# Kernel optimization log

Hardware: AMD Instinct MI355X
Metric: run time of the kernel (lower is better)

Reference implementation:

```python
import jax, jax.numpy as jnp
import numpy as np
import math

NUM_HEADS = 16


def setup_inputs() -> dict:
    key = jax.random.key(0)
    k0, k1, k2, k3, k4 = jax.random.split(key, 5)
    B, S, D = 2, 2048, 1024
    scale = 1.0 / math.sqrt(D)
    return {
        "x": jax.random.normal(k0, (B, S, D), dtype=jnp.float32),
        "Wq": jax.random.normal(k1, (D, D), dtype=jnp.float32) * scale,
        "Wk": jax.random.normal(k2, (D, D), dtype=jnp.float32) * scale,
        "Wv": jax.random.normal(k3, (D, D), dtype=jnp.float32) * scale,
        "Wo": jax.random.normal(k4, (D, D), dtype=jnp.float32) * scale,
    }


def reference(x, Wq, Wk, Wv, Wo):
    B, S, D = x.shape
    H = NUM_HEADS
    dk = D // H
    # nn.Linear(bias=False): y = x @ W.T; weights stored [out, in]
    def proj(W):
        return jnp.einsum('bsd,ed->bse', x, W).reshape(B, S, H, dk).transpose(0, 2, 1, 3)
    q = proj(Wq)  # [B, H, S, dk]
    k = proj(Wk)
    v = proj(Wv)
    scores = jnp.einsum('bhqd,bhkd->bhqk', q, k) / jnp.sqrt(jnp.float32(dk))
    causal = jnp.tril(jnp.ones((S, S), dtype=bool))  # True = keep
    scores = jnp.where(causal, scores, -jnp.inf)
    attn = jax.nn.softmax(scores, axis=-1)
    out = jnp.einsum('bhqk,bhkd->bhqd', attn, v)  # [B, H, S, dk]
    out = out.transpose(0, 2, 1, 3).reshape(B, S, D)
    return jnp.einsum('bsd,ed->bse', out, Wo)
```

## Files before the change

kernel.cpp:

```cpp
#include <hip/hip_runtime.h>
#include <hip/hip_bf16.h>

#define S_LEN 2048
#define S_PAD 2112
#define D_DIM 1024
#define N_HEADS 16
#define M_ROWS 4096

typedef __bf16 bf16x8 __attribute__((ext_vector_type(8)));
typedef float f32x4 __attribute__((ext_vector_type(4)));
typedef float f32x16 __attribute__((ext_vector_type(16)));
typedef unsigned short ushortx8 __attribute__((ext_vector_type(8)));
typedef unsigned int uintx4 __attribute__((ext_vector_type(4)));

__device__ __forceinline__ unsigned short f2bf(float f) {
  unsigned int u = __builtin_bit_cast(unsigned int, f);
  u += 0x7fffu + ((u >> 16) & 1u);
  return (unsigned short)(u >> 16);
}

__device__ __forceinline__ unsigned int cvtpk(float lo, float hi) {
  unsigned int r;
  asm("v_cvt_pk_bf16_f32 %0, %1, %2" : "=v"(r) : "v"(lo), "v"(hi));
  return r;
}

__device__ __forceinline__ void pl32swap(unsigned int& a, unsigned int& b) {
  asm("v_permlane32_swap_b32 %0, %1" : "+v"(a), "+v"(b));
}

__device__ __forceinline__ bf16x8 load8(const unsigned short* p) {
  return __builtin_bit_cast(bf16x8, *(const ushortx8*)p);
}

__device__ __forceinline__ void gload16(const unsigned short* g, unsigned short* l) {
  __builtin_amdgcn_global_load_lds((const __attribute__((address_space(1))) void*)g,
                                   (__attribute__((address_space(3))) void*)l,
                                   16, 0, 0);
}

__global__ void cvt5_kernel(const float* __restrict__ s0, const float* __restrict__ s1,
                            const float* __restrict__ s2, const float* __restrict__ s3,
                            const float* __restrict__ s4,
                            unsigned short* __restrict__ d0, unsigned short* __restrict__ d1,
                            unsigned short* __restrict__ d2, unsigned short* __restrict__ d3,
                            unsigned short* __restrict__ d4,
                            int n4x, int n4w) {
  const int y = blockIdx.y;
  const float* s = (y == 0) ? s0 : (y == 1) ? s1 : (y == 2) ? s2 : (y == 3) ? s3 : s4;
  unsigned short* d = (y == 0) ? d0 : (y == 1) ? d1 : (y == 2) ? d2 : (y == 3) ? d3 : d4;
  const int n4 = (y == 0) ? n4x : n4w;
  int i = blockIdx.x * blockDim.x + threadIdx.x;
  if (i < n4) {
    float4 f = ((const float4*)s)[i];
    unsigned int u0 = cvtpk(f.x, f.y), u1 = cvtpk(f.z, f.w);
    unsigned long long packed = (unsigned long long)u0 | ((unsigned long long)u1 << 32);
    ((unsigned long long*)d)[i] = packed;
  }
}

__global__ __launch_bounds__(256) void gemm_bt(
    const unsigned short* __restrict__ A,
    const unsigned short* __restrict__ B0,
    const unsigned short* __restrict__ B1,
    const unsigned short* __restrict__ B2,
    void* __restrict__ C0, void* __restrict__ C1, void* __restrict__ C2,
    int M, int N, int K, int modesel)
{
  __shared__ __align__(16) unsigned short At[128 * 64];
  __shared__ __align__(16) unsigned short Bt[128 * 64];

  const int bid = blockIdx.x + 8 * (blockIdx.y + 32 * blockIdx.z);
  const int k8 = bid & 7, t = bid >> 3;
  const int zz = t >> 5;
  const int u = t & 31;
  const int bxi = (k8 & 1) * 4 + (u & 3);
  const int byi = (k8 >> 1) * 8 + (u >> 2);

  const int z = zz;
  const unsigned short* Bp = (z == 0) ? B0 : (z == 1) ? B1 : B2;
  void* Cp = (z == 0) ? C0 : (z == 1) ? C1 : C2;
  const int mode = (modesel == 0) ? 0 : ((z == 2) ? 2 : 1);
  const float escale = (modesel == 1 && z == 0) ? 0.180336879f : 1.0f;

  const int tid = threadIdx.x;
  const int lane = tid & 63, wave = tid >> 6;
  const int bm = byi * 128, bn = bxi * 128;
  const int wr = wave >> 1, wc = wave & 1;
  const int cl = lane & 15, g = lane >> 4;
  const int ci = lane >> 3, si = lane & 7;
  const int sg = si ^ (ci & 7);

  f32x4 acc[4][4] = {};

  for (int kb = 0; kb < K; kb += 64) {
    __syncthreads();
#pragma unroll
    for (int cc = 0; cc < 4; ++cc) {
      int chunk = wave * 4 + cc;
      int row = chunk * 8 + ci;
      gload16(A  + (size_t)(bm + row) * K + kb + sg * 8, &At[chunk * 512]);
      gload16(Bp + (size_t)(bn + row) * K + kb + sg * 8, &Bt[chunk * 512]);
    }
    __syncthreads();
#pragma unroll
    for (int kc = 0; kc < 2; ++kc) {
      bf16x8 af[4], bfr[4];
#pragma unroll
      for (int mi = 0; mi < 4; ++mi) {
        int row = wr * 64 + mi * 16 + cl;
        int slot = (kc * 4 + g) ^ (row & 7);
        af[mi] = load8(&At[row * 64 + slot * 8]);
      }
#pragma unroll
      for (int ni = 0; ni < 4; ++ni) {
        int row = wc * 64 + ni * 16 + cl;
        int slot = (kc * 4 + g) ^ (row & 7);
        bfr[ni] = load8(&Bt[row * 64 + slot * 8]);
      }
#pragma unroll
      for (int mi = 0; mi < 4; ++mi)
#pragma unroll
        for (int ni = 0; ni < 4; ++ni)
          acc[mi][ni] = __builtin_amdgcn_mfma_f32_16x16x32_bf16(af[mi], bfr[ni], acc[mi][ni], 0, 0, 0);
    }
  }

  const int r0 = g * 4;
#pragma unroll
  for (int mi = 0; mi < 4; ++mi) {
#pragma unroll
    for (int ni = 0; ni < 4; ++ni) {
      int mg = bm + wr * 64 + mi * 16 + r0;
      int ng = bn + wc * 64 + ni * 16 + cl;
#pragma unroll
      for (int r = 0; r < 4; ++r) {
        float v = acc[mi][ni][r] * escale;
        int m = mg + r;
        if (mode == 0) {
          ((float*)Cp)[(size_t)m * N + ng] = v;
        } else {
          int b = m >> 11, s = m & 2047;
          int h = ng >> 6, d = ng & 63;
          unsigned short* o = (unsigned short*)Cp;
          if (mode == 1) o[((size_t)(b * N_HEADS + h) * S_LEN + s) * 64 + d] = f2bf(v);
          else           o[((size_t)(b * N_HEADS + h) * 64 + d) * S_PAD + s] = f2bf(v);
        }
      }
    }
  }
}

__global__ __launch_bounds__(256) void gemm_o64(
    const unsigned short* __restrict__ A,
    const unsigned short* __restrict__ B,
    float* __restrict__ C, int M, int N, int K)
{
  __shared__ __align__(16) unsigned short At[64 * 64];
  __shared__ __align__(16) unsigned short Bt[128 * 64];

  const int bid = blockIdx.x;
  const int k8 = bid & 7, t = bid >> 3;
  const int bxi = t & 7;
  const int byi = k8 * 8 + (t >> 3);

  const int tid = threadIdx.x;
  const int lane = tid & 63, wave = tid >> 6;
  const int bm = byi * 64, bn = bxi * 128;
  const int wr = wave >> 1, wc = wave & 1;
  const int cl = lane & 15, g = lane >> 4;
  const int ci = lane >> 3, si = lane & 7;
  const int sg = si ^ (ci & 7);

  f32x4 acc[2][4] = {};

  for (int kb = 0; kb < K; kb += 64) {
    __syncthreads();
#pragma unroll
    for (int cc = 0; cc < 2; ++cc) {
      int chunk = wave * 2 + cc;
      int row = chunk * 8 + ci;
      gload16(A + (size_t)(bm + row) * K + kb + sg * 8, &At[chunk * 512]);
    }
#pragma unroll
    for (int cc = 0; cc < 4; ++cc) {
      int chunk = wave * 4 + cc;
      int row = chunk * 8 + ci;
      gload16(B + (size_t)(bn + row) * K + kb + sg * 8, &Bt[chunk * 512]);
    }
    __syncthreads();
#pragma unroll
    for (int kc = 0; kc < 2; ++kc) {
      bf16x8 af[2], bfr[4];
#pragma unroll
      for (int mi = 0; mi < 2; ++mi) {
        int row = wr * 32 + mi * 16 + cl;
        int slot = (kc * 4 + g) ^ (row & 7);
        af[mi] = load8(&At[row * 64 + slot * 8]);
      }
#pragma unroll
      for (int ni = 0; ni < 4; ++ni) {
        int row = wc * 64 + ni * 16 + cl;
        int slot = (kc * 4 + g) ^ (row & 7);
        bfr[ni] = load8(&Bt[row * 64 + slot * 8]);
      }
#pragma unroll
      for (int mi = 0; mi < 2; ++mi)
#pragma unroll
        for (int ni = 0; ni < 4; ++ni)
          acc[mi][ni] = __builtin_amdgcn_mfma_f32_16x16x32_bf16(af[mi], bfr[ni], acc[mi][ni], 0, 0, 0);
    }
  }

  const int r0 = g * 4;
#pragma unroll
  for (int mi = 0; mi < 2; ++mi)
#pragma unroll
    for (int ni = 0; ni < 4; ++ni) {
      int mg = bm + wr * 32 + mi * 16 + r0;
      int ng = bn + wc * 64 + ni * 16 + cl;
#pragma unroll
      for (int r = 0; r < 4; ++r)
        C[(size_t)(mg + r) * N + ng] = acc[mi][ni][r];
    }
}

__global__ __launch_bounds__(256) void attn_kernel(
    const unsigned short* __restrict__ Qg,
    const unsigned short* __restrict__ Kg,
    const unsigned short* __restrict__ Vtg,
    unsigned short* __restrict__ Og)
{
  __shared__ __align__(16) unsigned short Kb[2][8192];
  __shared__ __align__(16) unsigned short Vb[2][8192];

  const int tid = threadIdx.x;
  const int lane = tid & 63, wave = tid >> 6;
  const int l31 = lane & 31, hi = lane >> 5;

  const int bh = (blockIdx.x & 7) * 4 + ((blockIdx.x >> 3) & 3);
  const int t  = 15 - (blockIdx.x >> 5);
  const int qt = t * 128;
  const size_t qkb = (size_t)bh * S_LEN;
  const int b = bh >> 4, h = bh & 15;

  int cur = 0;

  auto stageK = [&](int buf, int ch) {
    const unsigned short* base = Kg + (qkb + (size_t)ch * 128) * 64;
#pragma unroll
    for (int ii = 0; ii < 4; ++ii) {
      int i = wave * 4 + ii;
      int ri = i * 8 + (lane >> 3);
      int e = (((lane & 7) ^ (lane >> 3)) << 3);
      gload16(base + (size_t)ri * 64 + e, &Kb[buf][i * 512]);
    }
  };
  auto stageV = [&](int buf, int ch) {
    const unsigned short* base = Vtg + (size_t)bh * 64 * S_PAD + ch * 128;
#pragma unroll
    for (int ii = 0; ii < 4; ++ii) {
      int i = wave * 4 + ii;
      int ri = i * 4 + (lane >> 4);
      int e = (((lane & 15) ^ (ri & 7)) << 3);
      gload16(base + (size_t)ri * S_PAD + e, &Vb[buf][i * 512]);
    }
  };

  const int swz = (l31 & 7) << 3;

  auto kblock = [&](int buf, const bf16x8 (&bq)[4], f32x16 (&o)[2], float& lpart,
                    int j, int jj, bool domask, int qrow) {
    bf16x8 kc[4];
    int krow = j * 32 + l31;
#pragma unroll
    for (int f = 0; f < 4; ++f)
      kc[f] = load8(&Kb[buf][krow * 64 + ((f * 16 + hi * 8) ^ swz)]);
    f32x16 c = {};
    __builtin_amdgcn_s_setprio(1);
#pragma unroll
    for (int f = 0; f < 4; ++f)
      c = __builtin_amdgcn_mfma_f32_32x32x16_bf16(kc[f], bq[f], c, 0, 0, 0);
    __builtin_amdgcn_s_setprio(0);
    if (domask) {
#pragma unroll
      for (int r = 0; r < 16; ++r) {
        int k = jj * 32 + (r & 3) + 8 * (r >> 2) + 4 * hi;
        if (k > qrow) c[r] = -1e30f;
      }
    }
    float s0 = 0.f, s1 = 0.f;
#pragma unroll
    for (int r = 0; r < 16; r += 2) {
      c[r] = __builtin_amdgcn_exp2f(c[r]);         s0 += c[r];
      c[r + 1] = __builtin_amdgcn_exp2f(c[r + 1]); s1 += c[r + 1];
    }
    lpart += s0 + s1;
    bf16x8 pb[2];
#pragma unroll
    for (int kf = 0; kf < 2; ++kf) {
      unsigned int x0 = cvtpk(c[8 * kf + 0], c[8 * kf + 1]);
      unsigned int x1 = cvtpk(c[8 * kf + 2], c[8 * kf + 3]);
      unsigned int y0 = cvtpk(c[8 * kf + 4], c[8 * kf + 5]);
      unsigned int y1 = cvtpk(c[8 * kf + 6], c[8 * kf + 7]);
      pl32swap(x0, y0); pl32swap(x1, y1);
      pb[kf] = __builtin_bit_cast(bf16x8, (uintx4){x0, x1, y0, y1});
    }
    bf16x8 vf[2][2];
#pragma unroll
    for (int kf = 0; kf < 2; ++kf)
#pragma unroll
      for (int dt = 0; dt < 2; ++dt)
        vf[kf][dt] = load8(&Vb[buf][(dt * 32 + l31) * 128 + ((j * 32 + kf * 16 + hi * 8) ^ swz)]);
    __builtin_amdgcn_s_setprio(1);
#pragma unroll
    for (int kf = 0; kf < 2; ++kf)
#pragma unroll
      for (int dt = 0; dt < 2; ++dt)
        o[dt] = __builtin_amdgcn_mfma_f32_32x32x16_bf16(vf[kf][dt], pb[kf], o[dt], 0, 0, 0);
    __builtin_amdgcn_s_setprio(0);
  };

  bf16x8 bq[4];
#pragma unroll
  for (int f = 0; f < 4; ++f)
    bq[f] = load8(Qg + (qkb + qt + wave * 32 + l31) * 64 + f * 16 + hi * 8);

  f32x16 o[2] = {};
  float lpart = 0.f;
  const int qrow = qt + wave * 32 + l31;

  stageK(0, 0); stageV(0, 0);
  __syncthreads();

  for (int ch = 0; ch < t; ++ch) {
    stageK(cur ^ 1, ch + 1);
    stageV(cur ^ 1, ch + 1);
#pragma unroll
    for (int j = 0; j < 4; ++j)
      kblock(cur, bq, o, lpart, j, 0, false, 0);
    __syncthreads();
    cur ^= 1;
  }
  for (int j = 0; j <= wave; ++j)
    kblock(cur, bq, o, lpart, j, 4 * t + j, j == wave, qrow);

  {
    float lf = lpart + __shfl_xor(lpart, 32, 64);
    float inv = 1.0f / lf;
    unsigned short* base = Og + ((size_t)(b * S_LEN + qt + wave * 32 + l31)) * D_DIM
                         + h * 64 + 4 * hi;
#pragma unroll
    for (int dt = 0; dt < 2; ++dt)
#pragma unroll
      for (int rc = 0; rc < 4; ++rc) {
        unsigned int u0 = cvtpk(o[dt][4 * rc] * inv, o[dt][4 * rc + 1] * inv);
        unsigned int u1 = cvtpk(o[dt][4 * rc + 2] * inv, o[dt][4 * rc + 3] * inv);
        *(unsigned long long*)&base[dt * 32 + 8 * rc] =
            (unsigned long long)u0 | ((unsigned long long)u1 << 32);
      }
  }
}

extern "C" void kernel_launch(void* const* d_in, const int* in_sizes, int n_in,
                              void* d_out, int out_size, void* d_ws, size_t ws_size,
                              hipStream_t stream) {
  const float* x  = (const float*)d_in[0];
  const float* Wq = (const float*)d_in[1];
  const float* Wk = (const float*)d_in[2];
  const float* Wv = (const float*)d_in[3];
  const float* Wo = (const float*)d_in[4];

  const int M = M_ROWS, D = D_DIM;

  unsigned short* ws  = (unsigned short*)d_ws;
  unsigned short* xb  = ws;
  unsigned short* wqb = xb  + (size_t)M * D;
  unsigned short* wkb = wqb + (size_t)D * D;
  unsigned short* wvb = wkb + (size_t)D * D;
  unsigned short* wob = wvb + (size_t)D * D;
  unsigned short* qb  = wob + (size_t)D * D;
  unsigned short* kbf = qb  + (size_t)M * D;
  unsigned short* vtb = kbf + (size_t)M * D;
  unsigned short* aob = vtb + (size_t)32 * 64 * S_PAD;

  {
    dim3 gc(M * D / 4 / 256, 5);
    cvt5_kernel<<<gc, 256, 0, stream>>>(x, Wq, Wk, Wv, Wo,
                                        xb, wqb, wkb, wvb, wob,
                                        M * D / 4, D * D / 4);
  }

  dim3 gq(8, 32, 3);
  gemm_bt<<<gq, 256, 0, stream>>>(xb, wqb, wkb, wvb, qb, kbf, vtb, M, D, D, 1);

  attn_kernel<<<512, 256, 0, stream>>>(qb, kbf, vtb, aob);

  gemm_o64<<<512, 256, 0, stream>>>(aob, wob, (float*)d_out, M, D, D);
}
```

Before: 108.2 us.

## Double-buffer shared-memory tiles in projection and output GEMMs

Both GEMM kernels now keep two LDS buffers per operand and issue the global-to-LDS loads for the next K tile before computing on the current one. This cuts one barrier per iteration and aims to overlap load latency with MFMA work. It doubles LDS usage (64KB for gemm_bt), which may lower occupancy. Correctness depends on gload16 being a direct-to-LDS async load that completes by the single barrier at the end of each iteration.

Result: slower. 113.0 us (+4.4%).

```diff
diff --git a/kernel.cpp b/kernel.cpp
--- a/kernel.cpp
+++ b/kernel.cpp
@@ -67,8 +67,8 @@
     void* __restrict__ C0, void* __restrict__ C1, void* __restrict__ C2,
     int M, int N, int K, int modesel)
 {
-  __shared__ __align__(16) unsigned short At[128 * 64];
-  __shared__ __align__(16) unsigned short Bt[128 * 64];
+  __shared__ __align__(16) unsigned short At[2][128 * 64];
+  __shared__ __align__(16) unsigned short Bt[2][128 * 64];
 
   const int bid = blockIdx.x + 8 * (blockIdx.y + 32 * blockIdx.z);
   const int k8 = bid & 7, t = bid >> 3;
@@ -93,16 +93,23 @@
 
   f32x4 acc[4][4] = {};
 
-  for (int kb = 0; kb < K; kb += 64) {
-    __syncthreads();
+  auto stage = [&](int buf, int kb) {
 #pragma unroll
     for (int cc = 0; cc < 4; ++cc) {
       int chunk = wave * 4 + cc;
       int row = chunk * 8 + ci;
-      gload16(A  + (size_t)(bm + row) * K + kb + sg * 8, &At[chunk * 512]);
-      gload16(Bp + (size_t)(bn + row) * K + kb + sg * 8, &Bt[chunk * 512]);
-    }
-    __syncthreads();
+      gload16(A  + (size_t)(bm + row) * K + kb + sg * 8, &At[buf][chunk * 512]);
+      gload16(Bp + (size_t)(bn + row) * K + kb + sg * 8, &Bt[buf][chunk * 512]);
+    }
+  };
+
+  const int nk = K >> 6;
+  int cur = 0;
+  stage(0, 0);
+  __syncthreads();
+
+  for (int it = 0; it < nk; ++it) {
+    if (it + 1 < nk) stage(cur ^ 1, (it + 1) << 6);
 #pragma unroll
     for (int kc = 0; kc < 2; ++kc) {
       bf16x8 af[4], bfr[4];
@@ -110,13 +117,13 @@
       for (int mi = 0; mi < 4; ++mi) {
         int row = wr * 64 + mi * 16 + cl;
         int slot = (kc * 4 + g) ^ (row & 7);
-        af[mi] = load8(&At[row * 64 + slot * 8]);
+        af[mi] = load8(&At[cur][row * 64 + slot * 8]);
       }
 #pragma unroll
       for (int ni = 0; ni < 4; ++ni) {
         int row = wc * 64 + ni * 16 + cl;
         int slot = (kc * 4 + g) ^ (row & 7);
-        bfr[ni] = load8(&Bt[row * 64 + slot * 8]);
+        bfr[ni] = load8(&Bt[cur][row * 64 + slot * 8]);
       }
 #pragma unroll
       for (int mi = 0; mi < 4; ++mi)
@@ -124,6 +131,8 @@
         for (int ni = 0; ni < 4; ++ni)
           acc[mi][ni] = __builtin_amdgcn_mfma_f32_16x16x32_bf16(af[mi], bfr[ni], acc[mi][ni], 0, 0, 0);
     }
+    __syncthreads();
+    cur ^= 1;
   }
 
   const int r0 = g * 4;
@@ -156,8 +165,8 @@
     const unsigned short* __restrict__ B,
     float* __restrict__ C, int M, int N, int K)
 {
-  __shared__ __align__(16) unsigned short At[64 * 64];
-  __shared__ __align__(16) unsigned short Bt[128 * 64];
+  __shared__ __align__(16) unsigned short At[2][64 * 64];
+  __shared__ __align__(16) unsigned short Bt[2][128 * 64];
 
   const int bid = blockIdx.x;
   const int k8 = bid & 7, t = bid >> 3;
@@ -174,21 +183,28 @@
 
   f32x4 acc[2][4] = {};
 
-  for (int kb = 0; kb < K; kb += 64) {
-    __syncthreads();
+  auto stage = [&](int buf, int kb) {
 #pragma unroll
     for (int cc = 0; cc < 2; ++cc) {
       int chunk = wave * 2 + cc;
       int row = chunk * 8 + ci;
-      gload16(A + (size_t)(bm + row) * K + kb + sg * 8, &At[chunk * 512]);
+      gload16(A + (size_t)(bm + row) * K + kb + sg * 8, &At[buf][chunk * 512]);
     }
 #pragma unroll
     for (int cc = 0; cc < 4; ++cc) {
       int chunk = wave * 4 + cc;
       int row = chunk * 8 + ci;
-      gload16(B + (size_t)(bn + row) * K + kb + sg * 8, &Bt[chunk * 512]);
-    }
-    __syncthreads();
+      gload16(B + (size_t)(bn + row) * K + kb + sg * 8, &Bt[buf][chunk * 512]);
+    }
+  };
+
+  const int nk = K >> 6;
+  int cur = 0;
+  stage(0, 0);
+  __syncthreads();
+
+  for (int it = 0; it < nk; ++it) {
+    if (it + 1 < nk) stage(cur ^ 1, (it + 1) << 6);
 #pragma unroll
     for (int kc = 0; kc < 2; ++kc) {
       bf16x8 af[2], bfr[4];
@@ -196,13 +212,13 @@
       for (int mi = 0; mi < 2; ++mi) {
         int row = wr * 32 + mi * 16 + cl;
         int slot = (kc * 4 + g) ^ (row & 7);
-        af[mi] = load8(&At[row * 64 + slot * 8]);
+        af[mi] = load8(&At[cur][row * 64 + slot * 8]);
       }
 #pragma unroll
       for (int ni = 0; ni < 4; ++ni) {
         int row = wc * 64 + ni * 16 + cl;
         int slot = (kc * 4 + g) ^ (row & 7);
-        bfr[ni] = load8(&Bt[row * 64 + slot * 8]);
+        bfr[ni] = load8(&Bt[cur][row * 64 + slot * 8]);
       }
 #pragma unroll
       for (int mi = 0; mi < 2; ++mi)
@@ -210,6 +226,8 @@
         for (int ni = 0; ni < 4; ++ni)
           acc[mi][ni] = __builtin_amdgcn_mfma_f32_16x16x32_bf16(af[mi], bfr[ni], acc[mi][ni], 0, 0, 0);
     }
+    __syncthreads();
+    cur ^= 1;
   }
 
   const int r0 = g * 4;
```
